# Kernel tuning notes

Measured on AMD Instinct MI355X. Metric: run time of the kernel, lower is better.

The kernel has to match this reference:

```python
import jax, jax.numpy as jnp
import numpy as np

RADIUS = 4
SIGMA_X = 4.0
SIGMA_I = 10.0
P = 64                      # patch_size
NS = 2 * RADIUS + 1         # neighborhood_size = 9
EPS = float(np.finfo(np.float64).eps)


def _dist_weights():
    # Faithful to torch: dist varies only along the LAST window axis
    # (torch `expand` of a 1-D tensor to (9,9,9) broadcasts along dim -1).
    d = jnp.arange(1, NS + 1) - (RADIUS + 1)          # -4..4
    dist3d = jnp.broadcast_to(3 * d ** 2, (NS, NS, NS)).astype(jnp.float32)
    mask = (dist3d <= RADIUS).astype(jnp.float32)
    return (mask * jnp.exp(-dist3d / SIGMA_X ** 2)).reshape(-1)  # (729,)


_OFFSETS = jnp.asarray(
    np.stack(np.meshgrid(np.arange(NS), np.arange(NS), np.arange(NS), indexing='ij'),
             axis=-1).reshape(-1, 3), dtype=jnp.int32)            # (729, 3)


def _forward(batch, preds):
    B = batch.shape[0]
    K = preds.shape[1]
    pad = [(0, 0), (0, 0), (RADIUS, RADIUS), (RADIUS, RADIUS), (RADIUS, RADIUS)]
    pb = jnp.pad(batch, pad, constant_values=EPS)   # [B,1,P+2r,P+2r,P+2r]
    pp = jnp.pad(preds, pad, constant_values=EPS)   # [B,K,P+2r,P+2r,P+2r]
    dw = _dist_weights()

    def body(carry, od):
        off, w_o = od
        num, den = carry
        img_win = jax.lax.dynamic_slice(pb, (0, 0, off[0], off[1], off[2]),
                                        (B, 1, P, P, P))
        # Gaussian intensity affinity * spatial weight for this offset
        w = jnp.exp(-(img_win - batch) ** 2 / SIGMA_I ** 2) * w_o   # [B,1,P,P,P]
        pred_win = jax.lax.dynamic_slice(pp, (0, 0, off[0], off[1], off[2]),
                                         (B, K, P, P, P))
        return (num + w * pred_win, den + w), None

    num0 = jnp.zeros((B, K, P, P, P), batch.dtype)
    den0 = jnp.zeros((B, 1, P, P, P), batch.dtype)
    (num_map, den_map), _ = jax.lax.scan(body, (num0, den0), (_OFFSETS, dw))

    # Faithful to torch broadcasting: preds[B,1,P,P,P] * map[B,P,P,P] -> [B,B,...],
    # i.e. each sample's preds are contracted with the batch-summed maps.
    num_s = num_map.sum(axis=0)          # [K,P,P,P]
    den_s = den_map.sum(axis=0)[0]       # [P,P,P]
    numerator = jnp.einsum('bkxyz,kxyz->bk', preds, num_s)
    denominator = jnp.einsum('bkxyz,xyz->bk', preds, den_s)
    loss = (numerator + EPS) / (denominator + EPS)   # [B,K]
    return K - loss.sum(axis=1)                      # [B]


def setup_inputs() -> dict:
    key = jax.random.key(0)
    k1, k2 = jax.random.split(key)
    batch = jax.random.uniform(k1, (4, 1, P, P, P), dtype=jnp.float32)
    preds = jax.random.uniform(k2, (4, 4, P, P, P), dtype=jnp.float32)
    return {"batch": batch, "preds": preds}


def reference(batch, preds):
    return _forward(batch, preds)
```

## Files before the change

### kernel.cpp

```cpp
#include <hip/hip_runtime.h>
#include <hip/hip_fp16.h>


constexpr int Pdim = 64;
constexpr int P3   = Pdim * Pdim * Pdim;
constexpr int NREP = 16;

#define EPSF 2.2204460492503131e-16f

constexpr float WZ1   = 0.8290291181804004f;
constexpr float K2F   = 0.014426950408889634f;
constexpr float C1F   = 0.02f;
constexpr float WFULL = 81.0f * (1.0f + 2.0f * WZ1);

__global__ __launch_bounds__(128)
void ncuts_passx(const float* __restrict__ batch, const float* __restrict__ preds,
                 __half2* __restrict__ U, __half2* __restrict__ A,
                 float* __restrict__ acc, unsigned* __restrict__ ticket) {
  const int t = threadIdx.x;
  if (blockIdx.x == 0 && blockIdx.y == 0 && blockIdx.z == 0) {
    acc[t * 4 + 0] = 0.f; acc[t * 4 + 1] = 0.f;
    acc[t * 4 + 2] = 0.f; acc[t * 4 + 3] = 0.f;
    if (t == 0) *ticket = 0u;
  }
  const int z = t & 63, yh = t >> 6;
  const int y = blockIdx.x * 2 + yh;
  const int b = blockIdx.y;
  const int X0 = 16 * (int)blockIdx.z - 4;
  const int lin = (y << 6) + z;
  const float* Ip = batch + b * P3 + lin;
  const float* Pp = preds + b * 4 * P3 + lin;
  __half2* Ub = U + (b * 5) * P3 + lin;
  __half2* Ab = A + b * P3 + lin;

  float w[10][9], sum[10];
#pragma unroll
  for (int f = 0; f < 10; ++f) {
    sum[f] = 0.f;
#pragma unroll
    for (int i = 0; i < 9; ++i) w[f][i] = 0.f;
  }

#pragma unroll
  for (int i = 0; i < 24; ++i) {
    const int x = X0 + i;
    float u[10];
    if ((unsigned)x < 64u) {
      float I = Ip[x << 12];
      float g = exp2f(-I * I * K2F);
#pragma unroll
      for (int c = 0; c < 4; ++c) {
        float p = Pp[c * P3 + (x << 12)];
        u[2 * c]     = g * p;
        u[2 * c + 1] = u[2 * c] * I;
      }
      u[8] = g; u[9] = g * I;
      if (i >= 4 && i < 20)
        Ab[x << 12] = __floats2half2_rn(g, g * I * C1F);
    } else {
#pragma unroll
      for (int f = 0; f < 10; ++f) u[f] = 0.f;
    }
    const int r = i % 9;
#pragma unroll
    for (int f = 0; f < 10; ++f) { sum[f] += u[f] - w[f][r]; w[f][r] = u[f]; }
    if (i >= 8) {
      const int xo = x - 4;
#pragma unroll
      for (int c = 0; c < 5; ++c)
        Ub[c * P3 + (xo << 12)] = __floats2half2_rn(sum[2 * c], sum[2 * c + 1]);
    }
  }
}

__global__ __launch_bounds__(256)
void ncuts_passyz(const __half2* __restrict__ U, __half2* __restrict__ V) {
  const int t = threadIdx.x;
  const int z = t & 63, xh = t >> 6;
  const int x = blockIdx.x * 4 + xh;
  const int pair = blockIdx.y;
  const int Y0 = 16 * (int)blockIdx.z - 4;
  const __half2* src = U + pair * P3 + (x << 12) + z;
  __half2* dst = V + pair * P3 + (x << 12) + z;

  float w0[9], w1[9];
#pragma unroll
  for (int i = 0; i < 9; ++i) { w0[i] = 0.f; w1[i] = 0.f; }
  float s0 = 0.f, s1 = 0.f;
#pragma unroll
  for (int i = 0; i < 24; ++i) {
    const int y = Y0 + i;
    float u0 = 0.f, u1 = 0.f;
    if ((unsigned)y < 64u) {
      float2 u = __half22float2(src[y << 6]);
      u0 = u.x; u1 = u.y;
    }
    const int r = i % 9;
    s0 += u0 - w0[r]; w0[r] = u0;
    s1 += u1 - w1[r]; w1[r] = u1;
    if (i >= 8) {
      float up0 = __shfl_up(s0, 1, 64),   up1 = __shfl_up(s1, 1, 64);
      float dn0 = __shfl_down(s0, 1, 64), dn1 = __shfl_down(s1, 1, 64);
      if (z == 0)  { up0 = 0.f; up1 = 0.f; }
      if (z == 63) { dn0 = 0.f; dn1 = 0.f; }
      float v0 = __builtin_fmaf(WZ1, up0 + dn0, s0);
      float v1 = __builtin_fmaf(WZ1, up1 + dn1, s1);
      dst[(y - 4) << 6] = __floats2half2_rn(v0, v1);
    }
  }
}

__global__ __launch_bounds__(256)
void ncuts_contract(const float* __restrict__ preds, const __half2* __restrict__ A,
                    const __half2* __restrict__ V, float* __restrict__ acc,
                    unsigned* __restrict__ ticket, float* __restrict__ out) {
  __shared__ float red[4][32];
  __shared__ int islast;
  const int t   = threadIdx.x;
  const int idx = blockIdx.x * 256 + t;
  const int v0  = idx << 1;
  const int z = v0 & 63, y = (v0 >> 6) & 63, x = v0 >> 12;

  float a0[4][2], a1[4][2], gsum[2] = {0.f, 0.f};
#pragma unroll
  for (int b = 0; b < 4; ++b) {
    float2 raw = *(const float2*)(A + b * P3 + v0);
    float2 f0 = __half22float2(__builtin_bit_cast(__half2, raw.x));
    float2 f1 = __half22float2(__builtin_bit_cast(__half2, raw.y));
    a0[b][0] = f0.x; a1[b][0] = f0.y;
    a0[b][1] = f1.x; a1[b][1] = f1.y;
    gsum[0] += f0.x; gsum[1] += f1.x;
  }

  float ns[4][2] = {{0.f,0.f},{0.f,0.f},{0.f,0.f},{0.f,0.f}};
  float ds[2] = {0.f, 0.f};
#pragma unroll
  for (int b = 0; b < 4; ++b) {
#pragma unroll
    for (int c = 0; c < 5; ++c) {
      float2 raw = *(const float2*)(V + (b * 5 + c) * P3 + v0);
      float2 u0 = __half22float2(__builtin_bit_cast(__half2, raw.x));
      float2 u1 = __half22float2(__builtin_bit_cast(__half2, raw.y));
      float zc0 = __builtin_fmaf(a0[b][0], u0.x, a1[b][0] * u0.y);
      float zc1 = __builtin_fmaf(a0[b][1], u1.x, a1[b][1] * u1.y);
      if (c < 4) { ns[c][0] += zc0; ns[c][1] += zc1; }
      else       { ds[0]    += zc0; ds[1]    += zc1; }
    }
  }
  float cx = 9.f - (float)max(0, 4 - x) - (float)max(0, x - 59);
  float cy = 9.f - (float)max(0, 4 - y) - (float)max(0, y - 59);
  float cz0 = 1.f + WZ1 * ((z > 0 ? 1.f : 0.f) + 1.f);
  float cz1 = 1.f + WZ1 * (1.f + (z + 1 < 63 ? 1.f : 0.f));
  ds[0] = __builtin_fmaf(gsum[0], WFULL - cx * cy * cz0, ds[0]);
  ds[1] = __builtin_fmaf(gsum[1], WFULL - cx * cy * cz1, ds[1]);

  float pn[16], pd[16];
#pragma unroll
  for (int b = 0; b < 4; ++b) {
#pragma unroll
    for (int k = 0; k < 4; ++k) {
      float2 p = *(const float2*)(preds + (b * 4 + k) * P3 + v0);
      pn[b * 4 + k] = p.x * ns[k][0] + p.y * ns[k][1];
      pd[b * 4 + k] = p.x * ds[0]    + p.y * ds[1];
    }
  }

#pragma unroll
  for (int i = 0; i < 16; ++i) {
#pragma unroll
    for (int off = 32; off > 0; off >>= 1) {
      pn[i] += __shfl_down(pn[i], off, 64);
      pd[i] += __shfl_down(pd[i], off, 64);
    }
  }
  const int wave = t >> 6, lane = t & 63;
  if (lane == 0) {
#pragma unroll
    for (int i = 0; i < 16; ++i) { red[wave][i] = pn[i]; red[wave][16 + i] = pd[i]; }
  }
  __syncthreads();
  if (t < 32) {
    float s = red[0][t] + red[1][t] + red[2][t] + red[3][t];
    atomicAdd(&acc[(blockIdx.x & (NREP - 1)) * 32 + t], s);
  }
  __syncthreads();
  if (t == 0) {
    unsigned done = atomicAdd(ticket, 1u);
    islast = (done == gridDim.x - 1);
  }
  __syncthreads();
  if (islast) {
    if (t < 32) {
      float n = 0.f;
      for (int r = 0; r < NREP; ++r) n += atomicAdd(&acc[r * 32 + t], 0.f);
      red[0][t] = n;
    }
    __syncthreads();
    if (t < 4) {
      float s = 0.f;
      for (int k = 0; k < 4; ++k)
        s += (red[0][t * 4 + k] + EPSF) / (red[0][16 + t * 4 + k] + EPSF);
      out[t] = 4.0f - s;
    }
  }
}

constexpr int Rxy = 4;
constexpr int TXf = 8, TYf = 8;
constexpr int ZLEN = 2;
constexpr int RGX = 16, RGY = 16, RGZ = 10;
constexpr int YPf = 17, ZPf = 11;

__global__ __launch_bounds__(256, 2)
void ncuts_mainf(const float* __restrict__ batch, const float* __restrict__ preds,
                 float* __restrict__ acc) {
  __shared__ float  sB[RGX][YPf][ZPf];
  __shared__ float4 sP[RGX][YPf][ZPf];
  __shared__ float  red[4][32];

  const int t = threadIdx.x;
  const int tx = t & 7, ty = (t >> 3) & 7, tzt = t >> 6;
  const int bx0 = blockIdx.x * TXf, by0 = blockIdx.y * TYf, bz0 = blockIdx.z * 8;
  const int x = bx0 + tx, y = by0 + ty, z0 = bz0 + tzt * ZLEN;
  const int zc = tzt * ZLEN;

  float  den[ZLEN];
  float4 num[ZLEN];
#pragma unroll
  for (int j = 0; j < ZLEN; ++j) { den[j] = 0.f; num[j] = make_float4(0.f, 0.f, 0.f, 0.f); }

  const float C1 = -0.014426950408889634f;
  const float LWZ1 = -0.27050531991668065f;

  for (int b = 0; b < 4; ++b) {
    __syncthreads();
    for (int idx = t; idx < RGX * RGY * RGZ; idx += 256) {
      int rz = idx % RGZ, rq = idx / RGZ, ry = rq % RGY, rx = rq / RGY;
      int gx = bx0 + rx - Rxy, gy = by0 + ry - Rxy, gz = bz0 + rz - 1;
      bool in = ((unsigned)gx < 64u) & ((unsigned)gy < 64u) & ((unsigned)gz < 64u);
      float v = EPSF; float4 pv = make_float4(EPSF, EPSF, EPSF, EPSF);
      if (in) {
        int gi = (gx * Pdim + gy) * Pdim + gz;
        v = batch[b * P3 + gi];
        const float* pp = preds + b * 4 * P3 + gi;
        pv.x = pp[0]; pv.y = pp[P3]; pv.z = pp[2 * P3]; pv.w = pp[3 * P3];
      }
      sB[rx][ry][rz] = v; sP[rx][ry][rz] = pv;
    }
    __syncthreads();

    float I0[ZLEN];
#pragma unroll
    for (int j = 0; j < ZLEN; ++j) I0[j] = sB[tx + Rxy][ty + Rxy][zc + 1 + j];

#pragma unroll 1
    for (int dy = 0; dy < 9; ++dy) {
#pragma unroll 3
      for (int dx = 0; dx < 9; ++dx) {
        const float*  cb = &sB[tx + dx][ty + dy][zc];
        const float4* cp = &sP[tx + dx][ty + dy][zc];
        float colB[ZLEN + 2]; float4 colP[ZLEN + 2];
#pragma unroll
        for (int j = 0; j < ZLEN + 2; ++j) { colB[j] = cb[j]; colP[j] = cp[j]; }
#pragma unroll
        for (int j = 0; j < ZLEN; ++j) {
#pragma unroll
          for (int dz = 0; dz < 3; ++dz) {
            float d = colB[j + dz] - I0[j];
            float arg = __builtin_fmaf(d * d, C1, (dz == 1) ? 0.f : LWZ1);
            float w = exp2f(arg);
            den[j] += w;
            float4 p = colP[j + dz];
            num[j].x = __builtin_fmaf(w, p.x, num[j].x);
            num[j].y = __builtin_fmaf(w, p.y, num[j].y);
            num[j].z = __builtin_fmaf(w, p.z, num[j].z);
            num[j].w = __builtin_fmaf(w, p.w, num[j].w);
          }
        }
      }
    }
  }

  float pn[16], pd[16];
#pragma unroll
  for (int i = 0; i < 16; ++i) { pn[i] = 0.f; pd[i] = 0.f; }
#pragma unroll
  for (int b = 0; b < 4; ++b) {
#pragma unroll
    for (int j = 0; j < ZLEN; ++j) {
      const float* pp = preds + b * 4 * P3 + ((x * Pdim + y) * Pdim + z0 + j);
      float nsv[4] = {num[j].x, num[j].y, num[j].z, num[j].w};
#pragma unroll
      for (int k = 0; k < 4; ++k) {
        float pv = pp[k * P3];
        pn[b * 4 + k] = __builtin_fmaf(pv, nsv[k], pn[b * 4 + k]);
        pd[b * 4 + k] = __builtin_fmaf(pv, den[j], pd[b * 4 + k]);
      }
    }
  }
#pragma unroll
  for (int i = 0; i < 16; ++i) {
#pragma unroll
    for (int off = 32; off > 0; off >>= 1) {
      pn[i] += __shfl_down(pn[i], off, 64);
      pd[i] += __shfl_down(pd[i], off, 64);
    }
  }
  const int wave = t >> 6, lane = t & 63;
  if (lane == 0) {
#pragma unroll
    for (int i = 0; i < 16; ++i) { red[wave][i] = pn[i]; red[wave][16 + i] = pd[i]; }
  }
  __syncthreads();
  if (t < 32) {
    float s = red[0][t] + red[1][t] + red[2][t] + red[3][t];
    int bid = blockIdx.x + 8 * (blockIdx.y + 8 * (int)blockIdx.z);
    atomicAdd(&acc[(bid & (NREP - 1)) * 32 + t], s);
  }
}

__global__ void ncuts_zero(float* __restrict__ acc) {
  int t = threadIdx.x;
  if (t < NREP * 32) acc[t] = 0.f;
}

__global__ void ncuts_final(const float* __restrict__ acc, float* __restrict__ out) {
  __shared__ float loss[16];
  int t = threadIdx.x;
  if (t < 16) {
    float n = 0.f, d = 0.f;
    for (int r = 0; r < NREP; ++r) { n += acc[r * 32 + t]; d += acc[r * 32 + 16 + t]; }
    loss[t] = (n + EPSF) / (d + EPSF);
  }
  __syncthreads();
  if (t < 4) {
    float s = loss[t * 4] + loss[t * 4 + 1] + loss[t * 4 + 2] + loss[t * 4 + 3];
    out[t] = 4.0f - s;
  }
}

extern "C" void kernel_launch(void* const* d_in, const int* in_sizes, int n_in,
                              void* d_out, int out_size, void* d_ws, size_t ws_size,
                              hipStream_t stream) {
  const float* batch = (const float*)d_in[0];
  const float* preds = (const float*)d_in[1];
  float* out = (float*)d_out;

  const size_t ub = (size_t)20 * P3 * sizeof(__half2);
  const size_t vb = ub;
  const size_t ab = (size_t)4 * P3 * sizeof(__half2);
  const size_t need = ub + vb + ab + 8192;
  if (ws_size >= need) {
    char* base = (char*)d_ws;
    __half2*  U      = (__half2*)(base + 256);
    __half2*  V      = (__half2*)(base + 256 + ub);
    __half2*  A      = (__half2*)(base + 256 + ub + vb);
    float*    acc    = (float*)(base + 512 + ub + vb + ab);
    unsigned* ticket = (unsigned*)(base + 512 + ub + vb + ab + 2048);
    hipLaunchKernelGGL(ncuts_passx, dim3(32, 4, 4), dim3(128), 0, stream,
                       batch, preds, U, A, acc, ticket);
    hipLaunchKernelGGL(ncuts_passyz, dim3(16, 20, 4), dim3(256), 0, stream, U, V);
    hipLaunchKernelGGL(ncuts_contract, dim3(512), dim3(256), 0, stream,
                       preds, A, V, acc, ticket, out);
  } else {
    float* acc = (float*)d_ws;
    hipLaunchKernelGGL(ncuts_zero, dim3(1), dim3(512), 0, stream, acc);
    hipLaunchKernelGGL(ncuts_mainf, dim3(8, 8, 8), dim3(256), 0, stream,
                       batch, preds, acc);
    hipLaunchKernelGGL(ncuts_final, dim3(1), dim3(64), 0, stream, acc, out);
  }
}
```

Before: 102.7 us.

## Split x-pass per channel pair and recompute affinity in contract instead of storing A

The x-direction box-filter pass now gives each block a single (batch, channel) pair over 80 grid slices, instead of having each thread carry all ten running sums. This cuts register pressure from the 10x9 ring buffers and raises the number of waves in flight. The intermediate A buffer is removed; the contract kernel recomputes the Gaussian intensity weights from the batch volume. The cost is that the batch intensity and its exp2 are now loaded and computed five times per voxel in pass x, and once more in the contract kernel.

```diff
diff --git a/kernel.cpp b/kernel.cpp
--- a/kernel.cpp
+++ b/kernel.cpp
@@ -13,63 +13,45 @@
 constexpr float C1F   = 0.02f;
 constexpr float WFULL = 81.0f * (1.0f + 2.0f * WZ1);
 
-__global__ __launch_bounds__(128)
+__global__ __launch_bounds__(256)
 void ncuts_passx(const float* __restrict__ batch, const float* __restrict__ preds,
-                 __half2* __restrict__ U, __half2* __restrict__ A,
-                 float* __restrict__ acc, unsigned* __restrict__ ticket) {
+                 __half2* __restrict__ U, float* __restrict__ acc,
+                 unsigned* __restrict__ ticket) {
   const int t = threadIdx.x;
   if (blockIdx.x == 0 && blockIdx.y == 0 && blockIdx.z == 0) {
-    acc[t * 4 + 0] = 0.f; acc[t * 4 + 1] = 0.f;
-    acc[t * 4 + 2] = 0.f; acc[t * 4 + 3] = 0.f;
+    acc[t] = 0.f; acc[t + 256] = 0.f;
     if (t == 0) *ticket = 0u;
   }
   const int z = t & 63, yh = t >> 6;
-  const int y = blockIdx.x * 2 + yh;
-  const int b = blockIdx.y;
+  const int y = blockIdx.x * 4 + yh;
+  const int pair = blockIdx.y;
+  const int b = pair / 5, c = pair - 5 * b;
+  const bool isden = (c == 4);
   const int X0 = 16 * (int)blockIdx.z - 4;
   const int lin = (y << 6) + z;
   const float* Ip = batch + b * P3 + lin;
-  const float* Pp = preds + b * 4 * P3 + lin;
-  __half2* Ub = U + (b * 5) * P3 + lin;
-  __half2* Ab = A + b * P3 + lin;
-
-  float w[10][9], sum[10];
-#pragma unroll
-  for (int f = 0; f < 10; ++f) {
-    sum[f] = 0.f;
-#pragma unroll
-    for (int i = 0; i < 9; ++i) w[f][i] = 0.f;
-  }
-
+  const float* Pp = isden ? Ip : preds + (b * 4 + c) * P3 + lin;
+  __half2* Uo = U + pair * P3 + lin;
+
+  float w0[9], w1[9];
+#pragma unroll
+  for (int i = 0; i < 9; ++i) { w0[i] = 0.f; w1[i] = 0.f; }
+  float s0 = 0.f, s1 = 0.f;
 #pragma unroll
   for (int i = 0; i < 24; ++i) {
     const int x = X0 + i;
-    float u[10];
+    float u0 = 0.f, u1 = 0.f;
     if ((unsigned)x < 64u) {
       float I = Ip[x << 12];
       float g = exp2f(-I * I * K2F);
-#pragma unroll
-      for (int c = 0; c < 4; ++c) {
-        float p = Pp[c * P3 + (x << 12)];
-        u[2 * c]     = g * p;
-        u[2 * c + 1] = u[2 * c] * I;
-      }
-      u[8] = g; u[9] = g * I;
-      if (i >= 4 && i < 20)
-        Ab[x << 12] = __floats2half2_rn(g, g * I * C1F);
-    } else {
-#pragma unroll
-      for (int f = 0; f < 10; ++f) u[f] = 0.f;
+      float p = isden ? 1.f : Pp[x << 12];
+      u0 = g * p;
+      u1 = u0 * I;
     }
     const int r = i % 9;
-#pragma unroll
-    for (int f = 0; f < 10; ++f) { sum[f] += u[f] - w[f][r]; w[f][r] = u[f]; }
-    if (i >= 8) {
-      const int xo = x - 4;
-#pragma unroll
-      for (int c = 0; c < 5; ++c)
-        Ub[c * P3 + (xo << 12)] = __floats2half2_rn(sum[2 * c], sum[2 * c + 1]);
-    }
+    s0 += u0 - w0[r]; w0[r] = u0;
+    s1 += u1 - w1[r]; w1[r] = u1;
+    if (i >= 8) Uo[(x - 4) << 12] = __floats2half2_rn(s0, s1);
   }
 }
 
@@ -111,7 +93,7 @@
 }
 
 __global__ __launch_bounds__(256)
-void ncuts_contract(const float* __restrict__ preds, const __half2* __restrict__ A,
+void ncuts_contract(const float* __restrict__ batch, const float* __restrict__ preds,
                     const __half2* __restrict__ V, float* __restrict__ acc,
                     unsigned* __restrict__ ticket, float* __restrict__ out) {
   __shared__ float red[4][32];
@@ -124,12 +106,12 @@
   float a0[4][2], a1[4][2], gsum[2] = {0.f, 0.f};
 #pragma unroll
   for (int b = 0; b < 4; ++b) {
-    float2 raw = *(const float2*)(A + b * P3 + v0);
-    float2 f0 = __half22float2(__builtin_bit_cast(__half2, raw.x));
-    float2 f1 = __half22float2(__builtin_bit_cast(__half2, raw.y));
-    a0[b][0] = f0.x; a1[b][0] = f0.y;
-    a0[b][1] = f1.x; a1[b][1] = f1.y;
-    gsum[0] += f0.x; gsum[1] += f1.x;
+    float2 I = *(const float2*)(batch + b * P3 + v0);
+    float g0 = exp2f(-I.x * I.x * K2F);
+    float g1 = exp2f(-I.y * I.y * K2F);
+    a0[b][0] = g0; a1[b][0] = g0 * I.x * C1F;
+    a0[b][1] = g1; a1[b][1] = g1 * I.y * C1F;
+    gsum[0] += g0; gsum[1] += g1;
   }
 
   float ns[4][2] = {{0.f,0.f},{0.f,0.f},{0.f,0.f},{0.f,0.f}};
@@ -348,20 +330,18 @@
 
   const size_t ub = (size_t)20 * P3 * sizeof(__half2);
   const size_t vb = ub;
-  const size_t ab = (size_t)4 * P3 * sizeof(__half2);
-  const size_t need = ub + vb + ab + 8192;
+  const size_t need = ub + vb + 8192;
   if (ws_size >= need) {
     char* base = (char*)d_ws;
     __half2*  U      = (__half2*)(base + 256);
     __half2*  V      = (__half2*)(base + 256 + ub);
-    __half2*  A      = (__half2*)(base + 256 + ub + vb);
-    float*    acc    = (float*)(base + 512 + ub + vb + ab);
-    unsigned* ticket = (unsigned*)(base + 512 + ub + vb + ab + 2048);
-    hipLaunchKernelGGL(ncuts_passx, dim3(32, 4, 4), dim3(128), 0, stream,
-                       batch, preds, U, A, acc, ticket);
+    float*    acc    = (float*)(base + 512 + ub + vb);
+    unsigned* ticket = (unsigned*)(base + 512 + ub + vb + 2048);
+    hipLaunchKernelGGL(ncuts_passx, dim3(16, 20, 4), dim3(256), 0, stream,
+                       batch, preds, U, acc, ticket);
     hipLaunchKernelGGL(ncuts_passyz, dim3(16, 20, 4), dim3(256), 0, stream, U, V);
     hipLaunchKernelGGL(ncuts_contract, dim3(512), dim3(256), 0, stream,
-                       preds, A, V, acc, ticket, out);
+                       batch, preds, V, acc, ticket, out);
   } else {
     float* acc = (float*)d_ws;
     hipLaunchKernelGGL(ncuts_zero, dim3(1), dim3(512), 0, stream, acc);
```

After: 102.2 us. About the same (-0.5%).
